# Optimization experiments

Hardware: AMD Instinct MI355X
Metric: run time of the kernel (lower is better)

## Reference

```python
import jax, jax.numpy as jnp
import numpy as np
from jax import lax

B = 32768

def setup_inputs() -> dict:
    key = jax.random.key(0)
    ks = jax.random.split(key, 8)
    return {
        "x": jax.random.normal(ks[0], (B, 784), dtype=jnp.float32),
        "w_conv": jax.random.normal(ks[1], (3, 3), dtype=jnp.float32),
        "W1": jax.random.normal(ks[2], (676, 100), dtype=jnp.float32) * 0.05,
        "b1": jax.random.normal(ks[3], (100,), dtype=jnp.float32) * 0.05,
        "W2": jax.random.normal(ks[4], (100, 100), dtype=jnp.float32) * 0.05,
        "b2": jax.random.normal(ks[5], (100,), dtype=jnp.float32) * 0.05,
        "W3": jax.random.normal(ks[6], (100, 10), dtype=jnp.float32) * 0.05,
        "b3": jax.random.normal(ks[7], (10,), dtype=jnp.float32) * 0.05,
    }


def reference(x, w_conv, W1, b1, W2, b2, W3, b3):
    # x: [B, 784] -> [B, 1, 28, 28]; valid 3x3 cross-correlation (tensordot == correlation)
    xr = x.reshape(-1, 1, 28, 28)
    k = w_conv.reshape(1, 1, 3, 3)  # [out_c, in_c, kh, kw]
    conv = lax.conv_general_dilated(
        xr, k, window_strides=(1, 1), padding="VALID",
        dimension_numbers=("NCHW", "OIHW", "NCHW"))  # [B, 1, 26, 26]
    h = conv.reshape(conv.shape[0], 26 * 26)  # [B, 676]
    h = jax.nn.relu(h @ W1 + b1)
    h = jax.nn.relu(h @ W2 + b2)
    return h @ W3 + b3  # [B, 10]
```

## Files before the change

kernel.cpp:

```cpp
#include <hip/hip_runtime.h>


typedef __attribute__((ext_vector_type(8))) short bf16x8;
typedef __attribute__((ext_vector_type(4))) float f32x4;

#define KP1 832
#define NP  112
#define NPB 128
#define K2P 128
#define BM  64
#define NT  256

#define W2T_OFF (NPB * KP1)
#define W3T_OFF (W2T_OFF + NP * K2P)
#define WS_USHORTS (W3T_OFF + 16 * K2P)

#define WAITV4 asm volatile("s_waitcnt vmcnt(4)" ::: "memory")
#define WAITV0 asm volatile("s_waitcnt vmcnt(0)" ::: "memory")
#define BAR    __builtin_amdgcn_s_barrier()

__device__ __forceinline__ unsigned short f2bf(float f) {
    unsigned int u = __float_as_uint(f);
    u += 0x7FFFu + ((u >> 16) & 1u);
    return (unsigned short)(u >> 16);
}

__device__ __forceinline__ unsigned int pkbf(float a, float b) {
    unsigned int r;
    asm("v_cvt_pk_bf16_f32 %0, %1, %2" : "=v"(r) : "v"(a), "v"(b));
    return r;
}

__device__ __forceinline__ bf16x8 cvt8(float4 a, float4 b) {
    union { unsigned int w[4]; bf16x8 v; } u;
    u.w[0] = pkbf(a.x, a.y);
    u.w[1] = pkbf(a.z, a.w);
    u.w[2] = pkbf(b.x, b.y);
    u.w[3] = pkbf(b.z, b.w);
    return u.v;
}

__device__ __forceinline__ void gload_lds16(const void* g, void* l) {
    __builtin_amdgcn_global_load_lds(
        (const __attribute__((address_space(1))) unsigned int*)g,
        (__attribute__((address_space(3))) unsigned int*)l, 16, 0, 0);
}

__global__ void build_weights(const float* __restrict__ w_conv,
                              const float* __restrict__ W1,
                              const float* __restrict__ W2,
                              const float* __restrict__ W3,
                              unsigned short* __restrict__ ws) {
    const int idx = blockIdx.x * 256 + threadIdx.x;
    if (idx >= WS_USHORTS) return;
    float v = 0.f;
    if (idx < W2T_OFF) {
        const int col = idx / KP1, p = idx % KP1;
        if (col < 100 && p < 784) {
            const int y = p / 28, xx = p % 28;
#pragma unroll
            for (int ky = 0; ky < 3; ++ky) {
                const int py = y - ky;
                if (py < 0 || py >= 26) continue;
#pragma unroll
                for (int kx = 0; kx < 3; ++kx) {
                    const int px = xx - kx;
                    if (px < 0 || px >= 26) continue;
                    v += w_conv[ky * 3 + kx] * W1[(py * 26 + px) * 100 + col];
                }
            }
        }
    } else if (idx < W3T_OFF) {
        const int r = idx - W2T_OFF;
        const int col = r / K2P, k = r % K2P;
        if (col < 100 && k < 100) v = W2[k * 100 + col];
    } else {
        const int r = idx - W3T_OFF;
        const int col = r / K2P, k = r % K2P;
        if (col < 10 && k < 100) v = W3[k * 10 + col];
    }
    ws[idx] = f2bf(v);
}

__global__ __launch_bounds__(NT, 2)
void fused(const float* __restrict__ x,
           const unsigned short* __restrict__ wst,
           const float* __restrict__ b1,
           const float* __restrict__ b2,
           const float* __restrict__ b3,
           float* __restrict__ out) {
    __shared__ __attribute__((aligned(16))) float          xs[3][64][32];
    __shared__ __attribute__((aligned(16))) unsigned short bs[3][128][32];
    __shared__ __attribute__((aligned(16))) unsigned short h1[64][136];
    unsigned short (*h2)[136] = reinterpret_cast<unsigned short(*)[136]>(&xs[0][0][0]);

    const int tid  = threadIdx.x;
    const int lane = tid & 63;
    const int wv   = tid >> 6;
    const int l15  = lane & 15;
    const int lk   = lane >> 4;
    const int b0   = blockIdx.x * BM;
    const int wr   = wv * 16;

    const unsigned short* weff = wst;
    const unsigned short* w2t  = wst + W2T_OFF;
    const unsigned short* w3t  = wst + W3T_OFF;

    for (int f = lane; f < 16 * 14; f += 64) {
        const int r = wr + f / 14, c = 100 + (f % 14) * 2;
        *reinterpret_cast<unsigned int*>(&h1[r][c]) = 0u;
    }

    f32x4 acc[7];
#pragma unroll
    for (int n = 0; n < 7; ++n) acc[n] = (f32x4){0.f, 0.f, 0.f, 0.f};

    const int xrow_l = lane >> 3;
    const int xcol_b = (((lane & 7) ^ xrow_l) * 16);
    const int brow_l = lane >> 2;
    const int bcol_b = (((lane & 3) ^ (brow_l & 3)) * 16);

    auto issue = [&](int kt, float* xb, unsigned short* bb) {
#pragma unroll
        for (int q = 0; q < 2; ++q) {
            const int r = wr + 8 * q + xrow_l;
            const char* g = (const char*)(x + (size_t)(b0 + r) * 784 + kt * 32) + xcol_b;
            gload_lds16(g, (void*)(xb + (size_t)(wr + 8 * q) * 32));
        }
#pragma unroll
        for (int q = 0; q < 2; ++q) {
            const int r = wv * 32 + 16 * q + brow_l;
            const char* g = (const char*)(weff + (size_t)r * KP1 + kt * 32) + bcol_b;
            gload_lds16(g, (void*)(bb + (size_t)(wv * 32 + 16 * q) * 32));
        }
    };

    auto computeStage = [&](const float* xb, const unsigned short* bb) {
        const int r = wr + l15;
        const char* ap = (const char*)(xb + (size_t)r * 32);
        const int sA = (r & 7) << 4;
        const float4 lo = *reinterpret_cast<const float4*>(ap + ((lk * 32) ^ sA));
        const float4 hi = *reinterpret_cast<const float4*>(ap + ((lk * 32 + 16) ^ sA));
        const bf16x8 af = cvt8(lo, hi);
#pragma unroll
        for (int n = 0; n < 7; ++n) {
            const int rn = n * 16 + l15;
            const char* bp = (const char*)(bb + (size_t)rn * 32);
            const bf16x8 bfr = *reinterpret_cast<const bf16x8*>(bp + ((lk * 16) ^ ((rn & 3) << 4)));
            acc[n] = __builtin_amdgcn_mfma_f32_16x16x32_bf16(af, bfr, acc[n], 0, 0, 0);
        }
    };

    float* X0 = &xs[0][0][0]; unsigned short* B0 = &bs[0][0][0];
    float* X1 = &xs[1][0][0]; unsigned short* B1 = &bs[1][0][0];
    float* X2 = &xs[2][0][0]; unsigned short* B2 = &bs[2][0][0];

    issue(0, X0, B0);
    issue(1, X1, B1);
    WAITV4; BAR;
#pragma unroll 1
    for (int tt = 0; tt < 7; ++tt) {
        const int t = tt * 3;
        issue(t + 2, X2, B2); computeStage(X0, B0); WAITV4; BAR;
        issue(t + 3, X0, B0); computeStage(X1, B1); WAITV4; BAR;
        issue(t + 4, X1, B1); computeStage(X2, B2); WAITV4; BAR;
    }
    issue(23, X2, B2); computeStage(X0, B0); WAITV4; BAR;
    computeStage(X1, B1); WAITV0; BAR;
    computeStage(X2, B2);

    {
        float4 t0 = (float4){0.f, 0.f, 0.f, 0.f}, t1 = t0;
        if (lk < 2) {
            const float* xp = x + (size_t)(b0 + wr + l15) * 784 + 768 + lk * 8;
            t0 = *reinterpret_cast<const float4*>(xp);
            t1 = *reinterpret_cast<const float4*>(xp + 4);
        }
        const bf16x8 aft = cvt8(t0, t1);
#pragma unroll
        for (int n = 0; n < 7; ++n) {
            const bf16x8 bft = *reinterpret_cast<const bf16x8*>(
                weff + (size_t)(n * 16 + l15) * KP1 + 768 + lk * 8);
            acc[n] = __builtin_amdgcn_mfma_f32_16x16x32_bf16(aft, bft, acc[n], 0, 0, 0);
        }
    }
    __syncthreads();

    float bias[7];
#pragma unroll
    for (int n = 0; n < 7; ++n) {
        const int c = n * 16 + l15;
        bias[n] = (c < 100) ? b1[c] : 0.f;
    }
#pragma unroll
    for (int n = 0; n < 7; ++n) {
        const int col = n * 16 + l15;
        if (col < 100)
#pragma unroll
            for (int q = 0; q < 4; ++q) {
                const float v = fmaxf(acc[n][q] + bias[n], 0.f);
                h1[wr + lk * 4 + q][col] = f2bf(v);
            }
    }
    for (int f = lane; f < 16 * 14; f += 64) {
        const int r = wr + f / 14, c = 100 + (f % 14) * 2;
        *reinterpret_cast<unsigned int*>(&h2[r][c]) = 0u;
    }
    __builtin_amdgcn_sched_barrier(0);

    f32x4 acc2[7];
#pragma unroll
    for (int n = 0; n < 7; ++n) acc2[n] = (f32x4){0.f, 0.f, 0.f, 0.f};
#pragma unroll
    for (int ks = 0; ks < 4; ++ks) {
        const int kb = ks * 32 + lk * 8;
        const bf16x8 af = *reinterpret_cast<const bf16x8*>(&h1[wr + l15][kb]);
#pragma unroll
        for (int n = 0; n < 7; ++n) {
            const bf16x8 bfr = *reinterpret_cast<const bf16x8*>(
                w2t + (size_t)(n * 16 + l15) * K2P + kb);
            acc2[n] = __builtin_amdgcn_mfma_f32_16x16x32_bf16(af, bfr, acc2[n], 0, 0, 0);
        }
    }

#pragma unroll
    for (int n = 0; n < 7; ++n) {
        const int c = n * 16 + l15;
        bias[n] = (c < 100) ? b2[c] : 0.f;
    }
#pragma unroll
    for (int n = 0; n < 7; ++n) {
        const int col = n * 16 + l15;
        if (col < 100)
#pragma unroll
            for (int q = 0; q < 4; ++q) {
                const float v = fmaxf(acc2[n][q] + bias[n], 0.f);
                h2[wr + lk * 4 + q][col] = f2bf(v);
            }
    }
    __builtin_amdgcn_sched_barrier(0);

    f32x4 acc3 = (f32x4){0.f, 0.f, 0.f, 0.f};
#pragma unroll
    for (int ks = 0; ks < 4; ++ks) {
        const int kb = ks * 32 + lk * 8;
        const bf16x8 bfr = *reinterpret_cast<const bf16x8*>(
            w3t + (size_t)l15 * K2P + kb);
        const bf16x8 af = *reinterpret_cast<const bf16x8*>(&h2[wr + l15][kb]);
        acc3 = __builtin_amdgcn_mfma_f32_16x16x32_bf16(af, bfr, acc3, 0, 0, 0);
    }

    if (l15 < 10) {
        const float bb = b3[l15];
#pragma unroll
        for (int q = 0; q < 4; ++q) {
            const int row = b0 + wr + lk * 4 + q;
            out[(size_t)row * 10 + l15] = acc3[q] + bb;
        }
    }
}

extern "C" void kernel_launch(void* const* d_in, const int* in_sizes, int n_in,
                              void* d_out, int out_size, void* d_ws, size_t ws_size,
                              hipStream_t stream) {
    const float* x      = (const float*)d_in[0];
    const float* w_conv = (const float*)d_in[1];
    const float* W1     = (const float*)d_in[2];
    const float* b1     = (const float*)d_in[3];
    const float* W2     = (const float*)d_in[4];
    const float* b2     = (const float*)d_in[5];
    const float* W3     = (const float*)d_in[6];
    const float* b3     = (const float*)d_in[7];
    float* out = (float*)d_out;
    unsigned short* ws = (unsigned short*)d_ws;

    build_weights<<<(WS_USHORTS + 255) / 256, 256, 0, stream>>>(w_conv, W1, W2, W3, ws);
    fused<<<32768 / BM, NT, 0, stream>>>(x, ws, b1, b2, b3, out);
}
```

Before: 40.13 us.

## Split N dimension across wave pairs with 512-thread blocks

Doubles the block to 8 waves and splits the layer-1 and layer-2 output columns between two waves per 16-row group (4 and 3 column tiles), so each wave has fewer accumulators. Async tile loads are spread over all 8 waves, one x and one weight load each, and the wait count drops to match. Layer boundaries now use full block barriers because h1/h2 are shared across waves. This is meant to raise occupancy and latency hiding, at the cost of more barriers, an uneven column split, and layer 3 computed redundantly by both waves of a pair.

Measured after the change: 40.77 us. About the same (+1.6%).

```diff
diff --git a/kernel.cpp b/kernel.cpp
--- a/kernel.cpp
+++ b/kernel.cpp
@@ -9,13 +9,13 @@
 #define NPB 128
 #define K2P 128
 #define BM  64
-#define NT  256
+#define NT  512
 
 #define W2T_OFF (NPB * KP1)
 #define W3T_OFF (W2T_OFF + NP * K2P)
 #define WS_USHORTS (W3T_OFF + 16 * K2P)
 
-#define WAITV4 asm volatile("s_waitcnt vmcnt(4)" ::: "memory")
+#define WAITV2 asm volatile("s_waitcnt vmcnt(2)" ::: "memory")
 #define WAITV0 asm volatile("s_waitcnt vmcnt(0)" ::: "memory")
 #define BAR    __builtin_amdgcn_s_barrier()
 
@@ -82,7 +82,7 @@
     ws[idx] = f2bf(v);
 }
 
-__global__ __launch_bounds__(NT, 2)
+__global__ __launch_bounds__(NT, 4)
 void fused(const float* __restrict__ x,
            const unsigned short* __restrict__ wst,
            const float* __restrict__ b1,
@@ -97,42 +97,32 @@
     const int tid  = threadIdx.x;
     const int lane = tid & 63;
     const int wv   = tid >> 6;
+    const int wv_m = wv >> 1;
+    const int wv_n = wv & 1;
+    const int nb   = wv_n * 4;
     const int l15  = lane & 15;
     const int lk   = lane >> 4;
     const int b0   = blockIdx.x * BM;
-    const int wr   = wv * 16;
+    const int wr   = wv_m * 16;
 
     const unsigned short* weff = wst;
     const unsigned short* w2t  = wst + W2T_OFF;
     const unsigned short* w3t  = wst + W3T_OFF;
 
-    for (int f = lane; f < 16 * 14; f += 64) {
-        const int r = wr + f / 14, c = 100 + (f % 14) * 2;
-        *reinterpret_cast<unsigned int*>(&h1[r][c]) = 0u;
-    }
-
-    f32x4 acc[7];
-#pragma unroll
-    for (int n = 0; n < 7; ++n) acc[n] = (f32x4){0.f, 0.f, 0.f, 0.f};
-
-    const int xrow_l = lane >> 3;
-    const int xcol_b = (((lane & 7) ^ xrow_l) * 16);
-    const int brow_l = lane >> 2;
-    const int bcol_b = (((lane & 3) ^ (brow_l & 3)) * 16);
+    f32x4 acc[4];
+#pragma unroll
+    for (int j = 0; j < 4; ++j) acc[j] = (f32x4){0.f, 0.f, 0.f, 0.f};
+
+    const int xrow = wv * 8 + (lane >> 3);
+    const char* xsrc = (const char*)(x + (size_t)(b0 + xrow) * 784)
+                     + (((lane & 7) ^ (xrow & 7)) << 4);
+    const int brow = wv * 16 + (lane >> 2);
+    const char* bsrc = (const char*)(weff + (size_t)brow * KP1)
+                     + (((lane & 3) ^ (brow & 3)) << 4);
 
     auto issue = [&](int kt, float* xb, unsigned short* bb) {
-#pragma unroll
-        for (int q = 0; q < 2; ++q) {
-            const int r = wr + 8 * q + xrow_l;
-            const char* g = (const char*)(x + (size_t)(b0 + r) * 784 + kt * 32) + xcol_b;
-            gload_lds16(g, (void*)(xb + (size_t)(wr + 8 * q) * 32));
-        }
-#pragma unroll
-        for (int q = 0; q < 2; ++q) {
-            const int r = wv * 32 + 16 * q + brow_l;
-            const char* g = (const char*)(weff + (size_t)r * KP1 + kt * 32) + bcol_b;
-            gload_lds16(g, (void*)(bb + (size_t)(wv * 32 + 16 * q) * 32));
-        }
+        gload_lds16(xsrc + (size_t)kt * 128, (void*)(xb + wv * 8 * 32));
+        gload_lds16(bsrc + (size_t)kt * 64,  (void*)(bb + wv * 16 * 32));
     };
 
     auto computeStage = [&](const float* xb, const unsigned short* bb) {
@@ -143,11 +133,15 @@
         const float4 hi = *reinterpret_cast<const float4*>(ap + ((lk * 32 + 16) ^ sA));
         const bf16x8 af = cvt8(lo, hi);
 #pragma unroll
-        for (int n = 0; n < 7; ++n) {
-            const int rn = n * 16 + l15;
-            const char* bp = (const char*)(bb + (size_t)rn * 32);
-            const bf16x8 bfr = *reinterpret_cast<const bf16x8*>(bp + ((lk * 16) ^ ((rn & 3) << 4)));
-            acc[n] = __builtin_amdgcn_mfma_f32_16x16x32_bf16(af, bfr, acc[n], 0, 0, 0);
+        for (int j = 0; j < 4; ++j) {
+            const int nf = nb + j;
+            if (nf < 7) {
+                const int rn = nf * 16 + l15;
+                const char* bp = (const char*)(bb + (size_t)rn * 32);
+                const bf16x8 bfr = *reinterpret_cast<const bf16x8*>(
+                    bp + ((lk * 16) ^ ((rn & 3) << 4)));
+                acc[j] = __builtin_amdgcn_mfma_f32_16x16x32_bf16(af, bfr, acc[j], 0, 0, 0);
+            }
         }
     };
 
@@ -157,15 +151,15 @@
 
     issue(0, X0, B0);
     issue(1, X1, B1);
-    WAITV4; BAR;
+    WAITV2; BAR;
 #pragma unroll 1
     for (int tt = 0; tt < 7; ++tt) {
         const int t = tt * 3;
-        issue(t + 2, X2, B2); computeStage(X0, B0); WAITV4; BAR;
-        issue(t + 3, X0, B0); computeStage(X1, B1); WAITV4; BAR;
-        issue(t + 4, X1, B1); computeStage(X2, B2); WAITV4; BAR;
-    }
-    issue(23, X2, B2); computeStage(X0, B0); WAITV4; BAR;
+        issue(t + 2, X2, B2); computeStage(X0, B0); WAITV2; BAR;
+        issue(t + 3, X0, B0); computeStage(X1, B1); WAITV2; BAR;
+        issue(t + 4, X1, B1); computeStage(X2, B2); WAITV2; BAR;
+    }
+    issue(23, X2, B2); computeStage(X0, B0); WAITV2; BAR;
     computeStage(X1, B1); WAITV0; BAR;
     computeStage(X2, B2);
 
@@ -178,67 +172,78 @@
         }
         const bf16x8 aft = cvt8(t0, t1);
 #pragma unroll
-        for (int n = 0; n < 7; ++n) {
-            const bf16x8 bft = *reinterpret_cast<const bf16x8*>(
-                weff + (size_t)(n * 16 + l15) * KP1 + 768 + lk * 8);
-            acc[n] = __builtin_amdgcn_mfma_f32_16x16x32_bf16(aft, bft, acc[n], 0, 0, 0);
+        for (int j = 0; j < 4; ++j) {
+            const int nf = nb + j;
+            if (nf < 7) {
+                const bf16x8 bft = *reinterpret_cast<const bf16x8*>(
+                    weff + (size_t)(nf * 16 + l15) * KP1 + 768 + lk * 8);
+                acc[j] = __builtin_amdgcn_mfma_f32_16x16x32_bf16(aft, bft, acc[j], 0, 0, 0);
+            }
         }
     }
     __syncthreads();
 
-    float bias[7];
-#pragma unroll
-    for (int n = 0; n < 7; ++n) {
-        const int c = n * 16 + l15;
-        bias[n] = (c < 100) ? b1[c] : 0.f;
-    }
-#pragma unroll
-    for (int n = 0; n < 7; ++n) {
-        const int col = n * 16 + l15;
-        if (col < 100)
+    float bias[4];
+#pragma unroll
+    for (int j = 0; j < 4; ++j) {
+        const int c = (nb + j) * 16 + l15;
+        bias[j] = (nb + j < 7 && c < 100) ? b1[c] : 0.f;
+    }
+#pragma unroll
+    for (int j = 0; j < 4; ++j) {
+        const int nf = nb + j;
+        const int col = nf * 16 + l15;
+        if (nf < 7 && col < 100)
 #pragma unroll
             for (int q = 0; q < 4; ++q) {
-                const float v = fmaxf(acc[n][q] + bias[n], 0.f);
+                const float v = fmaxf(acc[j][q] + bias[j], 0.f);
                 h1[wr + lk * 4 + q][col] = f2bf(v);
             }
     }
-    for (int f = lane; f < 16 * 14; f += 64) {
-        const int r = wr + f / 14, c = 100 + (f % 14) * 2;
-        *reinterpret_cast<unsigned int*>(&h2[r][c]) = 0u;
-    }
-    __builtin_amdgcn_sched_barrier(0);
-
-    f32x4 acc2[7];
-#pragma unroll
-    for (int n = 0; n < 7; ++n) acc2[n] = (f32x4){0.f, 0.f, 0.f, 0.f};
+    if (wv_n == 1) {
+        for (int f = lane; f < 16 * 14; f += 64) {
+            const int r = wr + f / 14, c = 100 + (f % 14) * 2;
+            *reinterpret_cast<unsigned int*>(&h1[r][c]) = 0u;
+            *reinterpret_cast<unsigned int*>(&h2[r][c]) = 0u;
+        }
+    }
+    __syncthreads();
+
+    f32x4 acc2[4];
+#pragma unroll
+    for (int j = 0; j < 4; ++j) acc2[j] = (f32x4){0.f, 0.f, 0.f, 0.f};
 #pragma unroll
     for (int ks = 0; ks < 4; ++ks) {
         const int kb = ks * 32 + lk * 8;
         const bf16x8 af = *reinterpret_cast<const bf16x8*>(&h1[wr + l15][kb]);
 #pragma unroll
-        for (int n = 0; n < 7; ++n) {
-            const bf16x8 bfr = *reinterpret_cast<const bf16x8*>(
-                w2t + (size_t)(n * 16 + l15) * K2P + kb);
-            acc2[n] = __builtin_amdgcn_mfma_f32_16x16x32_bf16(af, bfr, acc2[n], 0, 0, 0);
-        }
-    }
-
-#pragma unroll
-    for (int n = 0; n < 7; ++n) {
-        const int c = n * 16 + l15;
-        bias[n] = (c < 100) ? b2[c] : 0.f;
-    }
-#pragma unroll
-    for (int n = 0; n < 7; ++n) {
-        const int col = n * 16 + l15;
-        if (col < 100)
+        for (int j = 0; j < 4; ++j) {
+            const int nf = nb + j;
+            if (nf < 7) {
+                const bf16x8 bfr = *reinterpret_cast<const bf16x8*>(
+                    w2t + (size_t)(nf * 16 + l15) * K2P + kb);
+                acc2[j] = __builtin_amdgcn_mfma_f32_16x16x32_bf16(af, bfr, acc2[j], 0, 0, 0);
+            }
+        }
+    }
+
+#pragma unroll
+    for (int j = 0; j < 4; ++j) {
+        const int c = (nb + j) * 16 + l15;
+        bias[j] = (nb + j < 7 && c < 100) ? b2[c] : 0.f;
+    }
+#pragma unroll
+    for (int j = 0; j < 4; ++j) {
+        const int nf = nb + j;
+        const int col = nf * 16 + l15;
+        if (nf < 7 && col < 100)
 #pragma unroll
             for (int q = 0; q < 4; ++q) {
-                const float v = fmaxf(acc2[n][q] + bias[n], 0.f);
+                const float v = fmaxf(acc2[j][q] + bias[j], 0.f);
                 h2[wr + lk * 4 + q][col] = f2bf(v);
             }
     }
-    __builtin_amdgcn_sched_barrier(0);
+    __syncthreads();
 
     f32x4 acc3 = (f32x4){0.f, 0.f, 0.f, 0.f};
 #pragma unroll
@@ -250,7 +255,7 @@
         acc3 = __builtin_amdgcn_mfma_f32_16x16x32_bf16(af, bfr, acc3, 0, 0, 0);
     }
 
-    if (l15 < 10) {
+    if (wv_n == 0 && l15 < 10) {
         const float bb = b3[l15];
 #pragma unroll
         for (int q = 0; q < 4; ++q) {
```
